# Kernel optimization log

Hardware: AMD Instinct MI355X
Metric: run time of the kernel (lower is better)

The kernel has to match this reference:

```python
import jax, jax.numpy as jnp
import numpy as np

DIM = 1024
HEADS = 16
DIM_HEAD = 64
INNER = HEADS * DIM_HEAD
SCALE = DIM_HEAD ** -0.5


def setup_inputs() -> dict:
    key = jax.random.key(0)
    kx, kq, kk, kv, ko = jax.random.split(key, 5)
    B, N = 2, 2048
    s = DIM ** -0.5
    return {
        "x": jax.random.normal(kx, (B, N, DIM), dtype=jnp.float32),
        "Wq": jax.random.normal(kq, (DIM, INNER), dtype=jnp.float32) * s,
        "Wk": jax.random.normal(kk, (DIM, INNER), dtype=jnp.float32) * s,
        "Wv": jax.random.normal(kv, (DIM, INNER), dtype=jnp.float32) * s,
        "Wo": jax.random.normal(ko, (INNER, DIM), dtype=jnp.float32) * s,
    }


def reference(x, Wq, Wk, Wv, Wo):
    B, N, _ = x.shape
    # projections, split heads: b n (h d) -> b h n d
    def split(t):
        return t.reshape(B, N, HEADS, DIM_HEAD).transpose(0, 2, 1, 3)
    q = split(x @ Wq)
    k = split(x @ Wk)
    v = split(x @ Wv)
    # scores [B,H,N,N]
    dots = jnp.einsum("bhnd,bhmd->bhnm", q, k) * SCALE
    # causal mask: positions j > i masked
    causal = jnp.triu(jnp.ones((N, N), dtype=bool), k=1)
    dots = jnp.where(causal, -jnp.inf, dots)
    attn = jax.nn.softmax(dots, axis=-1)
    out = jnp.einsum("bhnm,bhmd->bhnd", attn, v)
    out = out.transpose(0, 2, 1, 3).reshape(B, N, INNER)
    return out @ Wo
```

## Files before the change

### kernel.cpp

```cpp
#include <hip/hip_runtime.h>

typedef unsigned short u16;
typedef unsigned int u32;
typedef __attribute__((ext_vector_type(8))) short short8;
typedef __attribute__((ext_vector_type(4))) short s16x4;
typedef __attribute__((ext_vector_type(4))) float f32x4;
typedef __attribute__((ext_vector_type(2))) u32 u32x2;

typedef const __attribute__((address_space(1))) void* gptr_t;
typedef __attribute__((address_space(3))) void* sptr_t;

#define N_SEQ 2048
#define DIM 1024
#define INNER 1024
#define NTOK 4096
#define QKV_LD 3072

__device__ __forceinline__ u16 f2b(float f) {
  union { float f; unsigned u; } v; v.f = f;
  unsigned r = v.u + 0x7fffu + ((v.u >> 16) & 1u);
  return (u16)(r >> 16);
}

__global__ __launch_bounds__(256) void cast_x_kernel(const float* __restrict__ src,
                                                     u16* __restrict__ dst) {
  const size_t i = (size_t)blockIdx.x * 256 + threadIdx.x;
  const f32x4* s = (const f32x4*)(src + i * 8);
  f32x4 a = s[0], b = s[1];
  short8 o;
#pragma unroll
  for (int j = 0; j < 4; ++j) { o[j] = (short)f2b(a[j]); o[4 + j] = (short)f2b(b[j]); }
  *(short8*)(dst + i * 8) = o;
}

__global__ __launch_bounds__(256) void transpose_cast_kernel(const float* __restrict__ src,
                                                             u16* __restrict__ dst) {
  __shared__ u16 tile[64][65];
  const int n0 = blockIdx.x * 64, k0 = blockIdx.y * 64;
  for (int i = threadIdx.x; i < 4096; i += 256) {
    const int r = i >> 6, c = i & 63;
    tile[r][c] = f2b(src[(size_t)(k0 + r) * 1024 + n0 + c]);
  }
  __syncthreads();
  for (int i = threadIdx.x; i < 4096; i += 256) {
    const int r = i >> 6, c = i & 63;
    dst[(size_t)(n0 + r) * 1024 + k0 + c] = tile[c][r];
  }
}

__global__ __launch_bounds__(256) void transpose_v_kernel(const u16* __restrict__ qkv,
                                                          u16* __restrict__ vt) {
  __shared__ u16 t[64][72];
  const int nt0 = blockIdx.x * 64;
  const int bh = blockIdx.y;
  const int b = bh >> 4, h = bh & 15;
  const u16* src = qkv + (size_t)b * N_SEQ * QKV_LD + 2048 + h * 64;
#pragma unroll
  for (int i = 0; i < 2; ++i) {
    const int cid = i * 256 + threadIdx.x;
    const int r = cid >> 3, c = (cid & 7) * 8;
    *(short8*)&t[r][c] = *(const short8*)(src + (size_t)(nt0 + r) * QKV_LD + c);
  }
  __syncthreads();
#pragma unroll
  for (int i = 0; i < 2; ++i) {
    const int cid = i * 256 + threadIdx.x;
    const int d = cid >> 3, c = (cid & 7) * 8;
    short8 v;
#pragma unroll
    for (int j = 0; j < 8; ++j) v[j] = t[c + j][d];
    *(short8*)(vt + ((size_t)bh * 64 + d) * N_SEQ + nt0 + c) = v;
  }
}

template <typename OutT>
__global__ __launch_bounds__(256) void gemm_tn(const u16* __restrict__ A,
                                               const u16* __restrict__ Bt,
                                               OutT* __restrict__ C,
                                               int M, int N, int K) {
  __shared__ u16 Al[128 * 64];
  __shared__ u16 Bl[128 * 64];
  const int tid = threadIdx.x;
  const int w = tid >> 6, lane = tid & 63;
  const int l15 = lane & 15, lg = lane >> 4;
  const int wr = w >> 1, wc = w & 1;
  const int m0 = blockIdx.y * 128, n0 = blockIdx.x * 128;

  f32x4 acc[4][4] = {};

  for (int k0 = 0; k0 < K; k0 += 64) {
#pragma unroll
    for (int i = 0; i < 4; ++i) {
      const int chunk = (w << 2) + i;
      const int e = (chunk << 9) + lane * 8;
      const int row = e >> 6, col = e & 63;
      const u16* ga = A + (size_t)(m0 + row) * K + k0 + col;
      __builtin_amdgcn_global_load_lds((gptr_t)ga, (sptr_t)(Al + (chunk << 9)), 16, 0, 0);
      const u16* gb = Bt + (size_t)(n0 + row) * K + k0 + col;
      __builtin_amdgcn_global_load_lds((gptr_t)gb, (sptr_t)(Bl + (chunk << 9)), 16, 0, 0);
    }
    __syncthreads();
#pragma unroll
    for (int kk = 0; kk < 2; ++kk) {
      short8 af[4], bf[4];
#pragma unroll
      for (int m = 0; m < 4; ++m)
        af[m] = *(const short8*)(Al + ((wr * 64 + m * 16 + l15) << 6) + kk * 32 + lg * 8);
#pragma unroll
      for (int n = 0; n < 4; ++n)
        bf[n] = *(const short8*)(Bl + ((wc * 64 + n * 16 + l15) << 6) + kk * 32 + lg * 8);
#pragma unroll
      for (int m = 0; m < 4; ++m)
#pragma unroll
        for (int n = 0; n < 4; ++n)
          acc[m][n] = __builtin_amdgcn_mfma_f32_16x16x32_bf16(af[m], bf[n], acc[m][n], 0, 0, 0);
    }
    __syncthreads();
  }

#pragma unroll
  for (int m = 0; m < 4; ++m)
#pragma unroll
    for (int n = 0; n < 4; ++n)
#pragma unroll
      for (int r = 0; r < 4; ++r) {
        const int row = m0 + wr * 64 + m * 16 + lg * 4 + r;
        const int col = n0 + wc * 64 + n * 16 + l15;
        const float v = acc[m][n][r];
        if constexpr (sizeof(OutT) == 2) C[(size_t)row * N + col] = (OutT)f2b(v);
        else                             C[(size_t)row * N + col] = (OutT)v;
      }
}

__global__ __launch_bounds__(256) void attn_kernel(const u16* __restrict__ qkv,
                                                   const u16* __restrict__ vt,
                                                   u16* __restrict__ attnb) {
  const int bh = blockIdx.x;
  const int qt = 31 - (int)blockIdx.y;
  const int b = bh >> 4, h = bh & 15;
  const int tid = threadIdx.x;
  const int lane = tid & 63, w = tid >> 6;
  const int l15 = lane & 15, lg = lane >> 4;
  const int q0 = qt * 64;
  const int qrow = q0 + w * 16 + l15;

  __shared__ u16 Kl[128 * 64];
  __shared__ u16 Vl[64 * 128];
  __shared__ u16 Pl[4][16][136];

  const u16* base  = qkv + (size_t)b * N_SEQ * QKV_LD;
  const u16* kbase = base + 1024 + h * 64;
  const u16* vbase = vt + (size_t)bh * 64 * N_SEQ;

  short8 aq[2];
  {
    const u16* qp = base + (size_t)qrow * QKV_LD + h * 64 + lg * 8;
    aq[0] = *(const short8*)qp;
    aq[1] = *(const short8*)(qp + 32);
  }

  f32x4 o[4] = {};
  float m_run = -3.0e38f, l_run = 0.f;
  const float kscale = 0.125f * 1.4426950408889634f;
  const int nt = (qt >> 1) + 1;
  const int wbase = tid & ~63;

  for (int jt = 0; jt < nt; ++jt) {
    const int kv0 = jt * 128;
    __syncthreads();
#pragma unroll
    for (int i = 0; i < 4; ++i) {
      const int cid = i * 256 + tid;
      const int krow = cid >> 3, kc = (cid & 7) ^ (krow & 7);
      const u16* ks = kbase + (size_t)(kv0 + krow) * QKV_LD + kc * 8;
      __builtin_amdgcn_global_load_lds((gptr_t)ks, (sptr_t)(Kl + (i * 256 + wbase) * 8), 16, 0, 0);
      const int vrow = cid >> 4, vc0 = cid & 15;
      const int vc = (vc0 & 8) | ((vc0 & 7) ^ (vrow & 7));
      const u16* vs = vbase + (size_t)vrow * N_SEQ + kv0 + vc * 8;
      __builtin_amdgcn_global_load_lds((gptr_t)vs, (sptr_t)(Vl + (i * 256 + wbase) * 8), 16, 0, 0);
    }
    __syncthreads();

    f32x4 p[8];
#pragma unroll
    for (int mf = 0; mf < 8; ++mf) {
      f32x4 acc = {};
#pragma unroll
      for (int ks = 0; ks < 2; ++ks) {
        const int row = mf * 16 + l15;
        const int ch = (ks * 4 + lg) ^ (row & 7);
        short8 ak = *(const short8*)(Kl + row * 64 + ch * 8);
        acc = __builtin_amdgcn_mfma_f32_16x16x32_bf16(ak, aq[ks], acc, 0, 0, 0);
      }
      p[mf] = acc;
    }

    if (jt == nt - 1) {
#pragma unroll
      for (int mf = 0; mf < 8; ++mf)
#pragma unroll
        for (int r = 0; r < 4; ++r)
          if (kv0 + mf * 16 + lg * 4 + r > qrow) p[mf][r] = -3.0e38f;
    }

    float mt = p[0][0];
#pragma unroll
    for (int mf = 0; mf < 8; ++mf)
#pragma unroll
      for (int r = 0; r < 4; ++r) mt = fmaxf(mt, p[mf][r]);
    mt = fmaxf(mt, __shfl_xor(mt, 16, 64));
    mt = fmaxf(mt, __shfl_xor(mt, 32, 64));
    const float mn = fmaxf(m_run, mt);
    const float sf = exp2f((m_run - mn) * kscale);
    m_run = mn;
    float psum = 0.f;
#pragma unroll
    for (int mf = 0; mf < 8; ++mf)
#pragma unroll
      for (int r = 0; r < 4; ++r) {
        const float e = exp2f((p[mf][r] - mn) * kscale);
        p[mf][r] = e;
        psum += e;
      }
    psum += __shfl_xor(psum, 16, 64);
    psum += __shfl_xor(psum, 32, 64);
    l_run = l_run * sf + psum;
#pragma unroll
    for (int mf = 0; mf < 4; ++mf) o[mf] *= sf;

#pragma unroll
    for (int mf = 0; mf < 8; ++mf) {
      u32 d0, d1;
      asm("v_cvt_pk_bf16_f32 %0, %1, %2" : "=v"(d0) : "v"(p[mf][0]), "v"(p[mf][1]));
      asm("v_cvt_pk_bf16_f32 %0, %1, %2" : "=v"(d1) : "v"(p[mf][2]), "v"(p[mf][3]));
      u32x2 dd = {d0, d1};
      *(u32x2*)&Pl[w][l15][mf * 16 + lg * 4] = dd;
    }
    asm volatile("s_waitcnt lgkmcnt(0)" ::: "memory");

    short8 ap[4];
#pragma unroll
    for (int ks = 0; ks < 4; ++ks)
      ap[ks] = *(const short8*)&Pl[w][l15][ks * 32 + lg * 8];

#pragma unroll
    for (int mf = 0; mf < 4; ++mf)
#pragma unroll
      for (int ks = 0; ks < 4; ++ks) {
        const int row = mf * 16 + l15;
        const int ch = ks * 4 + lg;
        const int csw = (ch & 8) | ((ch & 7) ^ (row & 7));
        short8 av = *(const short8*)(Vl + row * 128 + csw * 8);
        o[mf] = __builtin_amdgcn_mfma_f32_16x16x32_bf16(av, ap[ks], o[mf], 0, 0, 0);
      }
  }

  const float inv = 1.f / l_run;
#pragma unroll
  for (int mf = 0; mf < 4; ++mf) {
    s16x4 sv;
#pragma unroll
    for (int r = 0; r < 4; ++r) sv[r] = (short)f2b(o[mf][r] * inv);
    u16* op = attnb + ((size_t)b * N_SEQ + qrow) * INNER + h * 64 + mf * 16 + lg * 4;
    *(s16x4*)op = sv;
  }
}

extern "C" void kernel_launch(void* const* d_in, const int* in_sizes, int n_in,
                              void* d_out, int out_size, void* d_ws, size_t ws_size,
                              hipStream_t stream) {
  const float* x  = (const float*)d_in[0];
  const float* Wq = (const float*)d_in[1];
  const float* Wk = (const float*)d_in[2];
  const float* Wv = (const float*)d_in[3];
  const float* Wo = (const float*)d_in[4];
  float* out = (float*)d_out;

  u16* xb    = (u16*)d_ws;
  u16* wqkvt = xb    + (size_t)NTOK * DIM;
  u16* wot   = wqkvt + (size_t)3 * INNER * DIM;
  u16* qkv   = wot   + (size_t)DIM * INNER;
  u16* attnb = qkv   + (size_t)NTOK * QKV_LD;
  u16* vtb   = attnb + (size_t)NTOK * INNER;

  cast_x_kernel<<<dim3(NTOK * DIM / (256 * 8)), 256, 0, stream>>>(x, xb);
  transpose_cast_kernel<<<dim3(16, 16), 256, 0, stream>>>(Wq, wqkvt);
  transpose_cast_kernel<<<dim3(16, 16), 256, 0, stream>>>(Wk, wqkvt + (size_t)1024 * 1024);
  transpose_cast_kernel<<<dim3(16, 16), 256, 0, stream>>>(Wv, wqkvt + (size_t)2048 * 1024);
  transpose_cast_kernel<<<dim3(16, 16), 256, 0, stream>>>(Wo, wot);

  gemm_tn<u16><<<dim3(3072 / 128, 4096 / 128), 256, 0, stream>>>(xb, wqkvt, qkv, NTOK, 3072, DIM);
  transpose_v_kernel<<<dim3(32, 32), 256, 0, stream>>>(qkv, vtb);
  attn_kernel<<<dim3(32, 32), 256, 0, stream>>>(qkv, vtb, attnb);
  gemm_tn<float><<<dim3(1024 / 128, 4096 / 128), 256, 0, stream>>>(attnb, wot, out, NTOK, INNER, INNER);
}
```

Before: 153.2 us.

## Double attention query tile per wave and swizzle GEMM block order

The attention kernel now processes 128 query rows per block, with each wave computing two 16-row groups. K and V fragments read from shared memory are reused for both groups, halving K/V tile loads and LDS reads per query row. The GEMM block index is permuted across 8 groups to improve L2 locality on the multi-die chip. In exchange, register pressure rises, the attention grid shrinks, and causal work balance becomes coarser.

```diff
diff --git a/kernel.cpp b/kernel.cpp
--- a/kernel.cpp
+++ b/kernel.cpp
@@ -84,7 +84,11 @@
   const int w = tid >> 6, lane = tid & 63;
   const int l15 = lane & 15, lg = lane >> 4;
   const int wr = w >> 1, wc = w & 1;
-  const int m0 = blockIdx.y * 128, n0 = blockIdx.x * 128;
+  const int nwg = gridDim.x * gridDim.y;
+  int bid = blockIdx.y * gridDim.x + blockIdx.x;
+  bid = (bid & 7) * (nwg >> 3) + (bid >> 3);
+  const int bx = bid % gridDim.x, by = bid / gridDim.x;
+  const int m0 = by * 128, n0 = bx * 128;
 
   f32x4 acc[4][4] = {};
 
@@ -136,33 +140,34 @@
                                                    const u16* __restrict__ vt,
                                                    u16* __restrict__ attnb) {
   const int bh = blockIdx.x;
-  const int qt = 31 - (int)blockIdx.y;
+  const int qt = 15 - (int)blockIdx.y;
   const int b = bh >> 4, h = bh & 15;
   const int tid = threadIdx.x;
   const int lane = tid & 63, w = tid >> 6;
   const int l15 = lane & 15, lg = lane >> 4;
-  const int q0 = qt * 64;
-  const int qrow = q0 + w * 16 + l15;
+  const int q0 = qt * 128;
+  const int qrow0 = q0 + w * 32 + l15;
 
   __shared__ u16 Kl[128 * 64];
   __shared__ u16 Vl[64 * 128];
-  __shared__ u16 Pl[4][16][136];
+  __shared__ u16 Pl[4][2][16][136];
 
   const u16* base  = qkv + (size_t)b * N_SEQ * QKV_LD;
   const u16* kbase = base + 1024 + h * 64;
   const u16* vbase = vt + (size_t)bh * 64 * N_SEQ;
 
-  short8 aq[2];
-  {
-    const u16* qp = base + (size_t)qrow * QKV_LD + h * 64 + lg * 8;
-    aq[0] = *(const short8*)qp;
-    aq[1] = *(const short8*)(qp + 32);
-  }
-
-  f32x4 o[4] = {};
-  float m_run = -3.0e38f, l_run = 0.f;
+  short8 aq[2][2];
+#pragma unroll
+  for (int g = 0; g < 2; ++g) {
+    const u16* qp = base + (size_t)(qrow0 + g * 16) * QKV_LD + h * 64 + lg * 8;
+    aq[g][0] = *(const short8*)qp;
+    aq[g][1] = *(const short8*)(qp + 32);
+  }
+
+  f32x4 o[2][4] = {};
+  float m_run[2] = {-3.0e38f, -3.0e38f}, l_run[2] = {0.f, 0.f};
   const float kscale = 0.125f * 1.4426950408889634f;
-  const int nt = (qt >> 1) + 1;
+  const int nt = qt + 1;
   const int wbase = tid & ~63;
 
   for (int jt = 0; jt < nt; ++jt) {
@@ -181,67 +186,80 @@
     }
     __syncthreads();
 
-    f32x4 p[8];
+    f32x4 p[2][8];
 #pragma unroll
     for (int mf = 0; mf < 8; ++mf) {
-      f32x4 acc = {};
+      short8 ak[2];
 #pragma unroll
       for (int ks = 0; ks < 2; ++ks) {
         const int row = mf * 16 + l15;
         const int ch = (ks * 4 + lg) ^ (row & 7);
-        short8 ak = *(const short8*)(Kl + row * 64 + ch * 8);
-        acc = __builtin_amdgcn_mfma_f32_16x16x32_bf16(ak, aq[ks], acc, 0, 0, 0);
-      }
-      p[mf] = acc;
+        ak[ks] = *(const short8*)(Kl + row * 64 + ch * 8);
+      }
+#pragma unroll
+      for (int g = 0; g < 2; ++g) {
+        f32x4 acc = {};
+#pragma unroll
+        for (int ks = 0; ks < 2; ++ks)
+          acc = __builtin_amdgcn_mfma_f32_16x16x32_bf16(ak[ks], aq[g][ks], acc, 0, 0, 0);
+        p[g][mf] = acc;
+      }
     }
 
     if (jt == nt - 1) {
 #pragma unroll
+      for (int g = 0; g < 2; ++g)
+#pragma unroll
+        for (int mf = 0; mf < 8; ++mf)
+#pragma unroll
+          for (int r = 0; r < 4; ++r)
+            if (kv0 + mf * 16 + lg * 4 + r > qrow0 + g * 16) p[g][mf][r] = -3.0e38f;
+    }
+
+#pragma unroll
+    for (int g = 0; g < 2; ++g) {
+      float mt = p[g][0][0];
+#pragma unroll
       for (int mf = 0; mf < 8; ++mf)
 #pragma unroll
-        for (int r = 0; r < 4; ++r)
-          if (kv0 + mf * 16 + lg * 4 + r > qrow) p[mf][r] = -3.0e38f;
-    }
-
-    float mt = p[0][0];
-#pragma unroll
-    for (int mf = 0; mf < 8; ++mf)
-#pragma unroll
-      for (int r = 0; r < 4; ++r) mt = fmaxf(mt, p[mf][r]);
-    mt = fmaxf(mt, __shfl_xor(mt, 16, 64));
-    mt = fmaxf(mt, __shfl_xor(mt, 32, 64));
-    const float mn = fmaxf(m_run, mt);
-    const float sf = exp2f((m_run - mn) * kscale);
-    m_run = mn;
-    float psum = 0.f;
-#pragma unroll
-    for (int mf = 0; mf < 8; ++mf)
-#pragma unroll
-      for (int r = 0; r < 4; ++r) {
-        const float e = exp2f((p[mf][r] - mn) * kscale);
-        p[mf][r] = e;
-        psum += e;
-      }
-    psum += __shfl_xor(psum, 16, 64);
-    psum += __shfl_xor(psum, 32, 64);
-    l_run = l_run * sf + psum;
-#pragma unroll
-    for (int mf = 0; mf < 4; ++mf) o[mf] *= sf;
-
-#pragma unroll
-    for (int mf = 0; mf < 8; ++mf) {
-      u32 d0, d1;
-      asm("v_cvt_pk_bf16_f32 %0, %1, %2" : "=v"(d0) : "v"(p[mf][0]), "v"(p[mf][1]));
-      asm("v_cvt_pk_bf16_f32 %0, %1, %2" : "=v"(d1) : "v"(p[mf][2]), "v"(p[mf][3]));
-      u32x2 dd = {d0, d1};
-      *(u32x2*)&Pl[w][l15][mf * 16 + lg * 4] = dd;
+        for (int r = 0; r < 4; ++r) mt = fmaxf(mt, p[g][mf][r]);
+      mt = fmaxf(mt, __shfl_xor(mt, 16, 64));
+      mt = fmaxf(mt, __shfl_xor(mt, 32, 64));
+      const float mn = fmaxf(m_run[g], mt);
+      const float sf = exp2f((m_run[g] - mn) * kscale);
+      m_run[g] = mn;
+      float psum = 0.f;
+#pragma unroll
+      for (int mf = 0; mf < 8; ++mf)
+#pragma unroll
+        for (int r = 0; r < 4; ++r) {
+          const float e = exp2f((p[g][mf][r] - mn) * kscale);
+          p[g][mf][r] = e;
+          psum += e;
+        }
+      psum += __shfl_xor(psum, 16, 64);
+      psum += __shfl_xor(psum, 32, 64);
+      l_run[g] = l_run[g] * sf + psum;
+#pragma unroll
+      for (int mf = 0; mf < 4; ++mf) o[g][mf] *= sf;
+
+#pragma unroll
+      for (int mf = 0; mf < 8; ++mf) {
+        u32 d0, d1;
+        asm("v_cvt_pk_bf16_f32 %0, %1, %2" : "=v"(d0) : "v"(p[g][mf][0]), "v"(p[g][mf][1]));
+        asm("v_cvt_pk_bf16_f32 %0, %1, %2" : "=v"(d1) : "v"(p[g][mf][2]), "v"(p[g][mf][3]));
+        u32x2 dd = {d0, d1};
+        *(u32x2*)&Pl[w][g][l15][mf * 16 + lg * 4] = dd;
+      }
     }
     asm volatile("s_waitcnt lgkmcnt(0)" ::: "memory");
 
-    short8 ap[4];
-#pragma unroll
-    for (int ks = 0; ks < 4; ++ks)
-      ap[ks] = *(const short8*)&Pl[w][l15][ks * 32 + lg * 8];
+    short8 ap[2][4];
+#pragma unroll
+    for (int g = 0; g < 2; ++g)
+#pragma unroll
+      for (int ks = 0; ks < 4; ++ks)
+        ap[g][ks] = *(const short8*)&Pl[w][g][l15][ks * 32 + lg * 8];
 
 #pragma unroll
     for (int mf = 0; mf < 4; ++mf)
@@ -251,18 +269,23 @@
         const int ch = ks * 4 + lg;
         const int csw = (ch & 8) | ((ch & 7) ^ (row & 7));
         short8 av = *(const short8*)(Vl + row * 128 + csw * 8);
-        o[mf] = __builtin_amdgcn_mfma_f32_16x16x32_bf16(av, ap[ks], o[mf], 0, 0, 0);
-      }
-  }
-
-  const float inv = 1.f / l_run;
-#pragma unroll
-  for (int mf = 0; mf < 4; ++mf) {
-    s16x4 sv;
-#pragma unroll
-    for (int r = 0; r < 4; ++r) sv[r] = (short)f2b(o[mf][r] * inv);
-    u16* op = attnb + ((size_t)b * N_SEQ + qrow) * INNER + h * 64 + mf * 16 + lg * 4;
-    *(s16x4*)op = sv;
+#pragma unroll
+        for (int g = 0; g < 2; ++g)
+          o[g][mf] = __builtin_amdgcn_mfma_f32_16x16x32_bf16(av, ap[g][ks], o[g][mf], 0, 0, 0);
+      }
+  }
+
+#pragma unroll
+  for (int g = 0; g < 2; ++g) {
+    const float inv = 1.f / l_run[g];
+#pragma unroll
+    for (int mf = 0; mf < 4; ++mf) {
+      s16x4 sv;
+#pragma unroll
+      for (int r = 0; r < 4; ++r) sv[r] = (short)f2b(o[g][mf][r] * inv);
+      u16* op = attnb + ((size_t)b * N_SEQ + qrow0 + g * 16) * INNER + h * 64 + mf * 16 + lg * 4;
+      *(s16x4*)op = sv;
+    }
   }
 }
 
@@ -291,6 +314,6 @@
 
   gemm_tn<u16><<<dim3(3072 / 128, 4096 / 128), 256, 0, stream>>>(xb, wqkvt, qkv, NTOK, 3072, DIM);
   transpose_v_kernel<<<dim3(32, 32), 256, 0, stream>>>(qkv, vtb);
-  attn_kernel<<<dim3(32, 32), 256, 0, stream>>>(qkv, vtb, attnb);
+  attn_kernel<<<dim3(32, 16), 256, 0, stream>>>(qkv, vtb, attnb);
   gemm_tn<float><<<dim3(1024 / 128, 4096 / 128), 256, 0, stream>>>(attnb, wot, out, NTOK, INNER, INNER);
 }
```

New measurement: 168.8 us. +10.2%, slower.

## Switch attention to 32x32 MFMA tiles with register-only P handoff

Applied to the files above, without the earlier changes.

The attention kernel now handles 128 query rows per block (32 per wave) using 32x32x16 bf16 MFMAs. The S^T accumulator is repacked into the B operand of the PV product with v_cvt_pk_bf16 and v_permlane32_swap, so the LDS round-trip for P goes away. The causal diagonal tile skips fully masked sub-blocks and the V LDS swizzle is widened to 16 chunks. Separately, the GEMM remaps block ids for better L2 locality. The trade is a halved attention grid with more registers per lane, which may reduce occupancy.

```diff
diff --git a/kernel.cpp b/kernel.cpp
--- a/kernel.cpp
+++ b/kernel.cpp
@@ -5,7 +5,8 @@
 typedef __attribute__((ext_vector_type(8))) short short8;
 typedef __attribute__((ext_vector_type(4))) short s16x4;
 typedef __attribute__((ext_vector_type(4))) float f32x4;
-typedef __attribute__((ext_vector_type(2))) u32 u32x2;
+typedef __attribute__((ext_vector_type(16))) float f32x16;
+typedef __attribute__((ext_vector_type(4))) u32 u32x4;
 
 typedef const __attribute__((address_space(1))) void* gptr_t;
 typedef __attribute__((address_space(3))) void* sptr_t;
@@ -84,7 +85,11 @@
   const int w = tid >> 6, lane = tid & 63;
   const int l15 = lane & 15, lg = lane >> 4;
   const int wr = w >> 1, wc = w & 1;
-  const int m0 = blockIdx.y * 128, n0 = blockIdx.x * 128;
+  const int nwg = gridDim.x * gridDim.y;
+  int bid = blockIdx.y * gridDim.x + blockIdx.x;
+  bid = (bid & 7) * (nwg >> 3) + (bid >> 3);
+  const int bx = bid % gridDim.x, by = bid / gridDim.x;
+  const int m0 = by * 128, n0 = bx * 128;
 
   f32x4 acc[4][4] = {};
 
@@ -136,33 +141,30 @@
                                                    const u16* __restrict__ vt,
                                                    u16* __restrict__ attnb) {
   const int bh = blockIdx.x;
-  const int qt = 31 - (int)blockIdx.y;
+  const int qt = 15 - (int)blockIdx.y;
   const int b = bh >> 4, h = bh & 15;
   const int tid = threadIdx.x;
   const int lane = tid & 63, w = tid >> 6;
-  const int l15 = lane & 15, lg = lane >> 4;
-  const int q0 = qt * 64;
-  const int qrow = q0 + w * 16 + l15;
+  const int l31 = lane & 31, hh = lane >> 5;
+  const int q0 = qt * 128;
+  const int qrow = q0 + w * 32 + l31;
 
   __shared__ u16 Kl[128 * 64];
   __shared__ u16 Vl[64 * 128];
-  __shared__ u16 Pl[4][16][136];
 
   const u16* base  = qkv + (size_t)b * N_SEQ * QKV_LD;
   const u16* kbase = base + 1024 + h * 64;
   const u16* vbase = vt + (size_t)bh * 64 * N_SEQ;
 
-  short8 aq[2];
-  {
-    const u16* qp = base + (size_t)qrow * QKV_LD + h * 64 + lg * 8;
-    aq[0] = *(const short8*)qp;
-    aq[1] = *(const short8*)(qp + 32);
-  }
-
-  f32x4 o[4] = {};
+  short8 bq[4];
+#pragma unroll
+  for (int ks = 0; ks < 4; ++ks)
+    bq[ks] = *(const short8*)(base + (size_t)qrow * QKV_LD + h * 64 + ks * 16 + hh * 8);
+
+  f32x16 o0 = {}, o1 = {};
   float m_run = -3.0e38f, l_run = 0.f;
   const float kscale = 0.125f * 1.4426950408889634f;
-  const int nt = (qt >> 1) + 1;
+  const int nt = qt + 1;
   const int wbase = tid & ~63;
 
   for (int jt = 0; jt < nt; ++jt) {
@@ -174,95 +176,107 @@
       const int krow = cid >> 3, kc = (cid & 7) ^ (krow & 7);
       const u16* ks = kbase + (size_t)(kv0 + krow) * QKV_LD + kc * 8;
       __builtin_amdgcn_global_load_lds((gptr_t)ks, (sptr_t)(Kl + (i * 256 + wbase) * 8), 16, 0, 0);
-      const int vrow = cid >> 4, vc0 = cid & 15;
-      const int vc = (vc0 & 8) | ((vc0 & 7) ^ (vrow & 7));
+      const int vrow = cid >> 4, vc = (cid & 15) ^ (vrow & 15);
       const u16* vs = vbase + (size_t)vrow * N_SEQ + kv0 + vc * 8;
       __builtin_amdgcn_global_load_lds((gptr_t)vs, (sptr_t)(Vl + (i * 256 + wbase) * 8), 16, 0, 0);
     }
     __syncthreads();
 
-    f32x4 p[8];
-#pragma unroll
-    for (int mf = 0; mf < 8; ++mf) {
-      f32x4 acc = {};
-#pragma unroll
-      for (int ks = 0; ks < 2; ++ks) {
-        const int row = mf * 16 + l15;
-        const int ch = (ks * 4 + lg) ^ (row & 7);
-        short8 ak = *(const short8*)(Kl + row * 64 + ch * 8);
-        acc = __builtin_amdgcn_mfma_f32_16x16x32_bf16(ak, aq[ks], acc, 0, 0, 0);
-      }
-      p[mf] = acc;
-    }
-
-    if (jt == nt - 1) {
-#pragma unroll
-      for (int mf = 0; mf < 8; ++mf)
-#pragma unroll
-        for (int r = 0; r < 4; ++r)
-          if (kv0 + mf * 16 + lg * 4 + r > qrow) p[mf][r] = -3.0e38f;
-    }
-
-    float mt = p[0][0];
-#pragma unroll
-    for (int mf = 0; mf < 8; ++mf)
-#pragma unroll
-      for (int r = 0; r < 4; ++r) mt = fmaxf(mt, p[mf][r]);
-    mt = fmaxf(mt, __shfl_xor(mt, 16, 64));
-    mt = fmaxf(mt, __shfl_xor(mt, 32, 64));
-    const float mn = fmaxf(m_run, mt);
-    const float sf = exp2f((m_run - mn) * kscale);
-    m_run = mn;
-    float psum = 0.f;
-#pragma unroll
-    for (int mf = 0; mf < 8; ++mf)
-#pragma unroll
-      for (int r = 0; r < 4; ++r) {
-        const float e = exp2f((p[mf][r] - mn) * kscale);
-        p[mf][r] = e;
-        psum += e;
-      }
-    psum += __shfl_xor(psum, 16, 64);
-    psum += __shfl_xor(psum, 32, 64);
-    l_run = l_run * sf + psum;
-#pragma unroll
-    for (int mf = 0; mf < 4; ++mf) o[mf] *= sf;
-
-#pragma unroll
-    for (int mf = 0; mf < 8; ++mf) {
-      u32 d0, d1;
-      asm("v_cvt_pk_bf16_f32 %0, %1, %2" : "=v"(d0) : "v"(p[mf][0]), "v"(p[mf][1]));
-      asm("v_cvt_pk_bf16_f32 %0, %1, %2" : "=v"(d1) : "v"(p[mf][2]), "v"(p[mf][3]));
-      u32x2 dd = {d0, d1};
-      *(u32x2*)&Pl[w][l15][mf * 16 + lg * 4] = dd;
-    }
-    asm volatile("s_waitcnt lgkmcnt(0)" ::: "memory");
-
-    short8 ap[4];
-#pragma unroll
-    for (int ks = 0; ks < 4; ++ks)
-      ap[ks] = *(const short8*)&Pl[w][l15][ks * 32 + lg * 8];
-
-#pragma unroll
-    for (int mf = 0; mf < 4; ++mf)
+    const bool last = (jt == nt - 1);
+#pragma unroll
+    for (int sub = 0; sub < 2; ++sub) {
+      if (last && sub == 1 && w < 2) continue;
+      const int kv0s = kv0 + sub * 64;
+
+      f32x16 p0 = {}, p1 = {};
 #pragma unroll
       for (int ks = 0; ks < 4; ++ks) {
-        const int row = mf * 16 + l15;
-        const int ch = ks * 4 + lg;
-        const int csw = (ch & 8) | ((ch & 7) ^ (row & 7));
-        short8 av = *(const short8*)(Vl + row * 128 + csw * 8);
-        o[mf] = __builtin_amdgcn_mfma_f32_16x16x32_bf16(av, ap[ks], o[mf], 0, 0, 0);
-      }
+        const int r0 = sub * 64 + l31;
+        const int r1 = r0 + 32;
+        short8 ak0 = *(const short8*)(Kl + r0 * 64 + (((ks * 2 + hh) ^ (r0 & 7)) * 8));
+        short8 ak1 = *(const short8*)(Kl + r1 * 64 + (((ks * 2 + hh) ^ (r1 & 7)) * 8));
+        p0 = __builtin_amdgcn_mfma_f32_32x32x16_bf16(ak0, bq[ks], p0, 0, 0, 0);
+        p1 = __builtin_amdgcn_mfma_f32_32x32x16_bf16(ak1, bq[ks], p1, 0, 0, 0);
+      }
+
+      if (last) {
+        const int kvb = kv0s + 4 * hh;
+#pragma unroll
+        for (int r = 0; r < 16; ++r) {
+          const int off = (r & 3) + 8 * (r >> 2);
+          if (kvb + off > qrow)      p0[r] = -3.0e38f;
+          if (kvb + 32 + off > qrow) p1[r] = -3.0e38f;
+        }
+      }
+
+      float mt = -3.0e38f;
+#pragma unroll
+      for (int r = 0; r < 16; ++r) { mt = fmaxf(mt, p0[r]); mt = fmaxf(mt, p1[r]); }
+      mt = fmaxf(mt, __shfl_xor(mt, 32, 64));
+      const float mn = fmaxf(m_run, mt);
+      const float sf = exp2f((m_run - mn) * kscale);
+      m_run = mn;
+      float ps = 0.f;
+#pragma unroll
+      for (int r = 0; r < 16; ++r) {
+        const float e0 = exp2f((p0[r] - mn) * kscale);
+        const float e1 = exp2f((p1[r] - mn) * kscale);
+        p0[r] = e0; p1[r] = e1;
+        ps += e0 + e1;
+      }
+      ps += __shfl_xor(ps, 32, 64);
+      l_run = l_run * sf + ps;
+      o0 *= sf; o1 *= sf;
+
+      u32 bpw[4][4];
+#define PACK_TILE(P, kf)                                                    \
+      {                                                                     \
+        _Pragma("unroll")                                                   \
+        for (int a2 = 0; a2 < 2; ++a2) {                                    \
+          _Pragma("unroll")                                                 \
+          for (int c2 = 0; c2 < 2; ++c2) {                                  \
+            u32 X, Y;                                                       \
+            asm("v_cvt_pk_bf16_f32 %0, %1, %2" : "=v"(X)                    \
+                : "v"(P[8 * a2 + 2 * c2]), "v"(P[8 * a2 + 2 * c2 + 1]));    \
+            asm("v_cvt_pk_bf16_f32 %0, %1, %2" : "=v"(Y)                    \
+                : "v"(P[8 * a2 + 4 + 2 * c2]), "v"(P[8 * a2 + 5 + 2 * c2]));\
+            asm("v_permlane32_swap_b32 %0, %1" : "+v"(X), "+v"(Y));         \
+            bpw[(kf) * 2 + a2][c2] = X;                   \
+            bpw[(kf) * 2 + a2][2 + c2] = Y;               \
+          }                                                                 \
+        }                                                                   \
+      }
+      PACK_TILE(p0, 0)
+      PACK_TILE(p1, 1)
+#undef PACK_TILE
+
+#pragma unroll
+      for (int ks16 = 0; ks16 < 4; ++ks16) {
+        u32x4 t = {bpw[ks16][0], bpw[ks16][1], bpw[ks16][2], bpw[ks16][3]};
+        short8 bp = __builtin_bit_cast(short8, t);
+        const int cb = sub * 8 + ks16 * 2 + hh;
+        const int row0 = l31;
+        const int row1 = 32 + l31;
+        short8 av0 = *(const short8*)(Vl + row0 * 128 + ((cb ^ (row0 & 15)) * 8));
+        short8 av1 = *(const short8*)(Vl + row1 * 128 + ((cb ^ (row1 & 15)) * 8));
+        o0 = __builtin_amdgcn_mfma_f32_32x32x16_bf16(av0, bp, o0, 0, 0, 0);
+        o1 = __builtin_amdgcn_mfma_f32_32x32x16_bf16(av1, bp, o1, 0, 0, 0);
+      }
+    }
   }
 
   const float inv = 1.f / l_run;
-#pragma unroll
-  for (int mf = 0; mf < 4; ++mf) {
-    s16x4 sv;
-#pragma unroll
-    for (int r = 0; r < 4; ++r) sv[r] = (short)f2b(o[mf][r] * inv);
-    u16* op = attnb + ((size_t)b * N_SEQ + qrow) * INNER + h * 64 + mf * 16 + lg * 4;
-    *(s16x4*)op = sv;
+  u16* orow = attnb + ((size_t)b * N_SEQ + qrow) * INNER + h * 64 + 4 * hh;
+#pragma unroll
+  for (int rq = 0; rq < 4; ++rq) {
+    s16x4 sv0, sv1;
+#pragma unroll
+    for (int j = 0; j < 4; ++j) {
+      sv0[j] = (short)f2b(o0[rq * 4 + j] * inv);
+      sv1[j] = (short)f2b(o1[rq * 4 + j] * inv);
+    }
+    *(s16x4*)(orow + rq * 8) = sv0;
+    *(s16x4*)(orow + 32 + rq * 8) = sv1;
   }
 }
 
@@ -291,6 +305,6 @@
 
   gemm_tn<u16><<<dim3(3072 / 128, 4096 / 128), 256, 0, stream>>>(xb, wqkvt, qkv, NTOK, 3072, DIM);
   transpose_v_kernel<<<dim3(32, 32), 256, 0, stream>>>(qkv, vtb);
-  attn_kernel<<<dim3(32, 32), 256, 0, stream>>>(qkv, vtb, attnb);
+  attn_kernel<<<dim3(32, 16), 256, 0, stream>>>(qkv, vtb, attnb);
   gemm_tn<float><<<dim3(1024 / 128, 4096 / 128), 256, 0, stream>>>(attnb, wot, out, NTOK, INNER, INNER);
 }
```

After: 158.8 us. 1.04x slower.
